# Performance work log

Hardware: AMD Instinct MI355X
Metric: run time of the kernel (lower is better)

The kernel has to match this reference:

```python
import jax, jax.numpy as jnp
import numpy as np

B_, L_, H_, P_ = 8, 4096, 512, 256
DT_MIN, DT_MAX = 1e-3, 1e-1


def setup_inputs() -> dict:
    key = jax.random.key(0)
    ks = jax.random.split(key, 6)
    input_sequence = jax.random.normal(ks[0], (B_, L_, H_), jnp.float32)
    # Stable diagonal SSM eigenvalues (HiPPO-like): negative real, spread imaginary
    Lambda_re = -0.5 * jnp.ones((P_,), jnp.float32)
    Lambda_im = jnp.pi * jnp.arange(P_, dtype=jnp.float32)
    # B, C stored as real arrays with trailing real/imag channel, as in the module
    B = jax.random.normal(ks[1], (P_, H_, 2), jnp.float32) / np.sqrt(2.0 * H_)
    C = jax.random.normal(ks[2], (H_, P_, 2), jnp.float32) / np.sqrt(float(P_))
    D = jax.random.normal(ks[3], (H_,), jnp.float32)
    log_step = jax.random.uniform(ks[4], (P_,), jnp.float32,
                                  float(np.log(DT_MIN)), float(np.log(DT_MAX)))
    return dict(input_sequence=input_sequence, Lambda_re=Lambda_re,
                Lambda_im=Lambda_im, B=B, C=C, D=D, log_step=log_step)


def _scan_ssm(Lambda_bar, Bu):
    """Diagonal linear recurrence x_k = Lambda_bar * x_{k-1} + Bu_k via parallel scan.
    Lambda_bar: (P,) complex64; Bu: (L, P) complex64 -> xs: (L, P) complex64."""
    A = jnp.broadcast_to(Lambda_bar, Bu.shape)

    def binop(e_i, e_j):
        a_i, b_i = e_i
        a_j, b_j = e_j
        return a_j * a_i, a_j * b_i + b_j

    _, xs = jax.lax.associative_scan(binop, (A, Bu))
    return xs


def reference(input_sequence, Lambda_re, Lambda_im, B, C, D, log_step):
    # complex parameters (conj_sym=True, clip_eigs=False, zoh discretization)
    Lambda = (Lambda_re + 1j * Lambda_im).astype(jnp.complex64)        # (P,)
    B_tilde = (B[..., 0] + 1j * B[..., 1]).astype(jnp.complex64)       # (P, H)
    C_tilde = (C[..., 0] + 1j * C[..., 1]).astype(jnp.complex64)       # (H, P)
    step = jnp.exp(log_step)                                           # (P,)
    # ZOH: Lambda_bar = exp(Lambda*dt); B_bar = Lambda^{-1}(Lambda_bar - I) B
    Lambda_bar = jnp.exp(Lambda * step)                                # (P,)
    B_bar = ((1.0 / Lambda) * (Lambda_bar - 1.0))[:, None] * B_tilde   # (P, H)
    # project inputs into state space: (B, L, P)
    Bu = jnp.einsum('blh,ph->blp', input_sequence.astype(jnp.complex64), B_bar)
    xs = jax.vmap(lambda bu: _scan_ssm(Lambda_bar, bu))(Bu)            # (B, L, P)
    state = xs[:, -1, :]                                               # (B, P)
    # conj_sym=True -> output uses 2 * Re(C x)
    ys = 2.0 * jnp.einsum('blp,hp->blh', xs, C_tilde).real             # (B, L, H)
    out = ys + D * input_sequence                                      # D-skip
    return out, state
```

## Files before the change

kernel.cpp:

```cpp
#include <hip/hip_runtime.h>
#include <hip/hip_bf16.h>

#define Hh 512
#define Pp 256
#define Ll 4096
#define Bb 8
#define BL (Bb*Ll)
#define Sc 64
#define NC 64

typedef __attribute__((ext_vector_type(8))) __bf16 bf16x8;
typedef __attribute__((ext_vector_type(4))) float  floatx4;

#define LAM_OFF     0
#define LAMS64D_OFF 512
#define B1G_OFF     1024
#define B3G_OFF     (B1G_OFF + 65536)
#define UB16_OFF    (B3G_OFF + 65536)
#define BUB_OFF     (UB16_OFF + 4194304)
#define XSB_OFF     (BUB_OFF + 4194304)
#define AGG_OFF     (XSB_OFF + 4194304)

#define OUT_ELEMS 16777216

#define GLL16(g, l) __builtin_amdgcn_global_load_lds( \
    (const __attribute__((address_space(1))) void*)(g), \
    (__attribute__((address_space(3))) void*)(l), 16, 0, 0)

#define BAR_LGKM()  asm volatile("s_waitcnt lgkmcnt(0)\n\ts_barrier" ::: "memory")
#define BAR_VMN(n)  asm volatile("s_waitcnt vmcnt(" #n ")\n\ts_barrier" ::: "memory")

__device__ __forceinline__ float2 cmul(float2 a, float2 b) {
    return make_float2(a.x*b.x - a.y*b.y, a.x*b.y + a.y*b.x);
}
__device__ __forceinline__ void cfma(float2& acc, float2 a, float2 b) {
    acc.x = fmaf(a.x, b.x, acc.x); acc.x = fmaf(-a.y, b.y, acc.x);
    acc.y = fmaf(a.x, b.y, acc.y); acc.y = fmaf( a.y, b.x, acc.y);
}

__global__ void prep(const float* __restrict__ u,
                     const float* __restrict__ Bmat, const float* __restrict__ Cmat,
                     const float* __restrict__ Lre, const float* __restrict__ Lim,
                     const float* __restrict__ logstep, float2* __restrict__ ws) {
    int bid = blockIdx.x;
    if (bid < 8192) {
        long i = ((long)bid * 256 + threadIdx.x) * 8;
        float4 v0 = *(const float4*)(u + i);
        float4 v1 = *(const float4*)(u + i + 4);
        __align__(16) __hip_bfloat162 t[4];
        t[0] = __float22bfloat162_rn(make_float2(v0.x, v0.y));
        t[1] = __float22bfloat162_rn(make_float2(v0.z, v0.w));
        t[2] = __float22bfloat162_rn(make_float2(v1.x, v1.y));
        t[3] = __float22bfloat162_rn(make_float2(v1.z, v1.w));
        *(bf16x8*)((__hip_bfloat16*)(ws + UB16_OFF) + i) = *(const bf16x8*)t;
    } else if (bid < 8704) {
        int idx = (bid - 8192) * 256 + threadIdx.x;
        int p = idx >> 9, h = idx & 511;
        double lr = (double)Lre[p], li = (double)Lim[p];
        double st = exp((double)logstep[p]);
        double a  = lr * st, th = li * st;
        double er = exp(a);
        double lamr = er * cos(th), lami = er * sin(th);
        double nr = lamr - 1.0, ni = lami;
        double den = lr*lr + li*li;
        float gx = (float)((nr*lr + ni*li)/den), gy = (float)((ni*lr - nr*li)/den);
        float2 b = ((const float2*)Bmat)[idx];
        float re = gx*b.x - gy*b.y;
        float im = gx*b.y + gy*b.x;
        __hip_bfloat16* B1 = (__hip_bfloat16*)(ws + B1G_OFF);
        B1[(2*p)*512 + h]   = __float2bfloat16(re);
        B1[(2*p+1)*512 + h] = __float2bfloat16(im);
    } else if (bid < 9216) {
        int idx = (bid - 8704) * 256 + threadIdx.x;
        int h = idx >> 8, p = idx & 255;
        float2 c = ((const float2*)Cmat)[idx];
        __hip_bfloat162* B3 = (__hip_bfloat162*)(ws + B3G_OFF);
        B3[h*256 + p] = __float22bfloat162_rn(make_float2(2.f*c.x, -2.f*c.y));
    } else {
        int p = threadIdx.x;
        double lr = (double)Lre[p], li = (double)Lim[p];
        double st = exp((double)logstep[p]);
        double a  = lr * st, th = li * st;
        double er = exp(a);
        ws[LAM_OFF + p] = make_float2((float)(er*cos(th)), (float)(er*sin(th)));
        double er64 = exp(64.0 * a), th64 = 64.0 * th;
        ((double2*)(ws + LAMS64D_OFF))[p] = make_double2(er64*cos(th64), er64*sin(th64));
    }
}

#define STAGE(buf, kt) do { \
    _Pragma("unroll") \
    for (int h_ = 0; h_ < 2; ++h_) { \
        _Pragma("unroll") \
        for (int r_ = 0; r_ < 2; ++r_) { \
            GLL16(aSrc + (h_*128 + r_*64)*1024 + (kt)*128, \
                  ldsSt + (buf)*65536 + h_*16384 + r_*8192); \
            GLL16(bSrc + (h_*128 + r_*64)*1024 + (kt)*128, \
                  ldsSt + (buf)*65536 + 32768 + h_*16384 + r_*8192); \
        } \
    } \
} while (0)

__global__ __launch_bounds__(512, 2)
void gemm1(const __hip_bfloat16* __restrict__ A,
           const __hip_bfloat16* __restrict__ B,
           void* __restrict__ Cout,
           const float2* __restrict__ lamTab,
           float2* __restrict__ aggOut) {
    __shared__ __align__(16) char lds[131072];
    const int tid = threadIdx.x;
    const int w = tid >> 6, l = tid & 63;

    const int idx = blockIdx.x;
    const int swz = (idx & 7) * 32 + (idx >> 3);
    const int mt = swz >> 1, nt = swz & 1;
    const long M0 = (long)mt * 256;
    const int  N0 = nt * 256;

    const int rA  = l >> 3;
    const int csw = ((l & 7) ^ rA) * 16;
    const char* aSrc = (const char*)A + (M0 + w*8 + rA) * 1024 + csw;
    const char* bSrc = (const char*)B + (long)(N0 + w*8 + rA) * 1024 + csw;
    char* ldsSt = lds + w*1024 + l*16;

    const int quad = l >> 4, ml = l & 15, m7 = ml & 7;
    const int wm = w & 1, wn = w >> 1;
    const int o0 = ((quad    ) ^ m7) * 16;
    const int o1 = ((quad + 4) ^ m7) * 16;
    const char* aRd = lds + wm*16384 + ml*128;
    const char* bRd = lds + 32768 + wn*8192 + ml*128;

    floatx4 acc[8][4];
    #pragma unroll
    for (int i = 0; i < 8; ++i)
        #pragma unroll
        for (int j = 0; j < 4; ++j) acc[i][j] = (floatx4)0.f;

    STAGE(0, 0);
    STAGE(1, 1);
    BAR_VMN(8);

    #pragma unroll
    for (int t = 0; t < 8; ++t) {
        const int tb = (t & 1) * 65536;
        {
            bf16x8 af[8], bfr[4];
            #pragma unroll
            for (int fm = 0; fm < 8; ++fm)
                af[fm] = *(const bf16x8*)(aRd + tb + fm*2048 + o0);
            #pragma unroll
            for (int fn = 0; fn < 4; ++fn)
                bfr[fn] = *(const bf16x8*)(bRd + tb + fn*2048 + o0);
            __builtin_amdgcn_s_setprio(1);
            #pragma unroll
            for (int fm = 0; fm < 8; ++fm)
                #pragma unroll
                for (int fn = 0; fn < 4; ++fn)
                    acc[fm][fn] = __builtin_amdgcn_mfma_f32_16x16x32_bf16(
                        af[fm], bfr[fn], acc[fm][fn], 0, 0, 0);
            __builtin_amdgcn_s_setprio(0);
        }
        {
            bf16x8 af[8], bfr[4];
            #pragma unroll
            for (int fm = 0; fm < 8; ++fm)
                af[fm] = *(const bf16x8*)(aRd + tb + fm*2048 + o1);
            #pragma unroll
            for (int fn = 0; fn < 4; ++fn)
                bfr[fn] = *(const bf16x8*)(bRd + tb + fn*2048 + o1);
            BAR_LGKM();
            if (t + 2 < 8) STAGE(t & 1, t + 2);
            __builtin_amdgcn_sched_barrier(0);
            __builtin_amdgcn_s_setprio(1);
            #pragma unroll
            for (int fm = 0; fm < 8; ++fm)
                #pragma unroll
                for (int fn = 0; fn < 4; ++fn)
                    acc[fm][fn] = __builtin_amdgcn_mfma_f32_16x16x32_bf16(
                        af[fm], bfr[fn], acc[fm][fn], 0, 0, 0);
            __builtin_amdgcn_s_setprio(0);
        }
        if (t < 6)       BAR_VMN(8);
        else if (t == 6) BAR_VMN(0);
    }

    const int b   = (int)(M0 >> 12);
    const int gc0 = (int)((M0 >> 6) & 63);
    #pragma unroll
    for (int fn = 0; fn < 4; ++fn) {
        const int col = N0 + wn*64 + fn*16 + ml;
        const int p = col >> 1;
        const float2 lam = lamTab[p];
        const float2 one = make_float2(1.f, 0.f);
        const float2 l2  = cmul(lam, lam);
        const float2 l3  = cmul(l2, lam);
        const float2 l4  = cmul(l2, l2);
        const float2 l8  = cmul(l4, l4);
        const float2 l12 = cmul(l8, l4);
        const float2 l16 = cmul(l8, l8);
        const float2 l32 = cmul(l16, l16);
        const float2 l48 = cmul(l32, l16);
        const float2 P4q = (quad==3) ? one : (quad==2) ? l4 : (quad==1) ? l8 : l12;
        #pragma unroll
        for (int c = 0; c < 2; ++c) {
            float2 sc = make_float2(0.f, 0.f);
            #pragma unroll
            for (int a = 0; a < 4; ++a) {
                const int fm = c*4 + a;
                float vr[4];
                #pragma unroll
                for (int reg = 0; reg < 4; ++reg) {
                    const long row = M0 + wm*128 + fm*16 + quad*4 + reg;
                    __hip_bfloat16 hv = __float2bfloat16(acc[fm][fn][reg]);
                    ((__hip_bfloat16*)Cout)[row * 512 + col] = hv;
                    vr[reg] = __bfloat162float(hv);
                }
                float2 s;
                s.x = fmaf(l3.x, vr[0], fmaf(l2.x, vr[1], fmaf(lam.x, vr[2], vr[3])));
                s.y = fmaf(l3.y, vr[0], fmaf(l2.y, vr[1], lam.y * vr[2]));
                const float2 p16 = (a==3) ? one : (a==2) ? l16 : (a==1) ? l32 : l48;
                cfma(sc, cmul(p16, P4q), s);
            }
            sc.x += __shfl_xor(sc.x, 16); sc.y += __shfl_xor(sc.y, 16);
            sc.x += __shfl_xor(sc.x, 32); sc.y += __shfl_xor(sc.y, 32);
            const float ox = __shfl_xor(sc.x, 1);
            const float oy = __shfl_xor(sc.y, 1);
            if (quad == 0 && (ml & 1) == 0) {
                aggOut[(b*NC + gc0 + wm*2 + c) * Pp + p] =
                    make_float2(sc.x - oy, sc.y + ox);
            }
        }
    }
}

#define STAGEB(buf, kt) do { \
    _Pragma("unroll") \
    for (int h_ = 0; h_ < 2; ++h_) { \
        _Pragma("unroll") \
        for (int r_ = 0; r_ < 2; ++r_) { \
            GLL16(bSrc + (h_*128 + r_*64)*1024 + (kt)*128, \
                  ldsB + (buf)*32768 + h_*16384 + r_*8192); \
        } \
    } \
} while (0)

__global__ __launch_bounds__(512, 2)
void gemm2f(const __hip_bfloat162* __restrict__ bub,
            const __hip_bfloat16* __restrict__ Bg,
            float* __restrict__ out,
            const __hip_bfloat16* __restrict__ ub,
            const float* __restrict__ Dv,
            const float2* __restrict__ lamTab,
            const double2* __restrict__ lam64,
            const float2* __restrict__ agg) {
    __shared__ __align__(16) char lds[139264];
    const int tid = threadIdx.x;
    const int w = tid >> 6, l = tid & 63;

    const int idx = blockIdx.x;
    const int swz = (idx & 7) * 32 + (idx >> 3);
    const int mt = swz >> 1, nt = swz & 1;
    const long M0 = (long)mt * 256;
    const int  N0 = nt * 256;
    const int b   = (int)(M0 >> 12);
    const int gc0 = (int)((M0 >> 6) & 63);

    const int rA  = l >> 3;
    const int csw = ((l & 7) ^ rA) * 16;
    const char* bSrc = (const char*)Bg + (long)(N0 + w*8 + rA) * 1024 + csw;
    char* ldsB = lds + 65536 + w*1024 + l*16;

    const int quad = l >> 4, ml = l & 15, m7 = ml & 7;
    const int wm = w & 1, wn = w >> 1;
    const int o0 = ((quad    ) ^ m7) * 16;
    const int o1 = ((quad + 4) ^ m7) * 16;
    const char* aRd = lds + wm*16384 + ml*128;
    const char* bRd = lds + 65536 + wn*8192 + ml*128;

    float2* carryL = (float2*)(lds + 131072);

    if (tid < 256) {
        const int p = tid;
        const double2 l64 = lam64[p];
        double cr = 0.0, ci = 0.0;
        for (int cp = 0; cp < gc0; ++cp) {
            float2 a = agg[(b*NC + cp) * Pp + p];
            double nr = fma(l64.x, cr, (double)a.x); nr = fma(-l64.y, ci, nr);
            double ni = fma(l64.x, ci, (double)a.y); ni = fma( l64.y, cr, ni);
            cr = nr; ci = ni;
        }
        carryL[0*256 + p] = make_float2((float)cr, (float)ci);
        #pragma unroll
        for (int i = 1; i < 4; ++i) {
            float2 a = agg[(b*NC + gc0 + i - 1) * Pp + p];
            double nr = fma(l64.x, cr, (double)a.x); nr = fma(-l64.y, ci, nr);
            double ni = fma(l64.x, ci, (double)a.y); ni = fma( l64.y, cr, ni);
            cr = nr; ci = ni;
            carryL[i*256 + p] = make_float2((float)cr, (float)ci);
        }
    }
    __syncthreads();

    floatx4 acc[8][4];
    #pragma unroll
    for (int i = 0; i < 8; ++i)
        #pragma unroll
        for (int j = 0; j < 4; ++j) acc[i][j] = (floatx4)0.f;

    auto scanTile = [&](int kt, int bufA) {
        if (tid < 128) {
            const int p5 = tid & 31, chunk = tid >> 5;
            const int p = kt*32 + p5;
            const float2 lam = lamTab[p];
            float2 x = carryL[chunk*256 + p];
            const __hip_bfloat162* src = bub + ((long)(M0 + chunk*64)) * 256 + p;
            char* abase = lds + bufA*32768 + (chunk*64)*128;
            const int cs = p5*4;
            for (int j0 = 0; j0 < 64; j0 += 8) {
                float2 v[8];
                #pragma unroll
                for (int i = 0; i < 8; ++i)
                    v[i] = __bfloat1622float2(src[(long)(j0 + i) * 256]);
                #pragma unroll
                for (int i = 0; i < 8; ++i) {
                    float nr = fmaf(lam.x, x.x, v[i].x); nr = fmaf(-lam.y, x.y, nr);
                    float ni = fmaf(lam.x, x.y, v[i].y); ni = fmaf( lam.y, x.x, ni);
                    x.x = nr; x.y = ni;
                    const int j = j0 + i;
                    *(__hip_bfloat162*)(abase + j*128 + (cs ^ ((j & 7) << 4))) =
                        __float22bfloat162_rn(x);
                }
            }
            if (gc0 == 60 && chunk == 3 && nt == 0) {
                out[OUT_ELEMS + b * Pp + p] = x.x;
                out[OUT_ELEMS + Bb * Pp + b * Pp + p] = x.y;
            }
        }
    };

    scanTile(0, 0);
    STAGEB(0, 0);
    __syncthreads();

    for (int kt = 0; kt < 8; ++kt) {
        const int cb = kt & 1;
        if (kt < 7) { scanTile(kt + 1, cb ^ 1); STAGEB(cb ^ 1, kt + 1); }
        __syncthreads();
        const int tb = cb * 32768;
        bf16x8 af[8], bfr[4];
        #pragma unroll
        for (int fm = 0; fm < 8; ++fm)
            af[fm] = *(const bf16x8*)(aRd + tb + fm*2048 + o0);
        #pragma unroll
        for (int fn = 0; fn < 4; ++fn)
            bfr[fn] = *(const bf16x8*)(bRd + tb + fn*2048 + o0);
        __builtin_amdgcn_s_setprio(1);
        #pragma unroll
        for (int fm = 0; fm < 8; ++fm)
            #pragma unroll
            for (int fn = 0; fn < 4; ++fn)
                acc[fm][fn] = __builtin_amdgcn_mfma_f32_16x16x32_bf16(
                    af[fm], bfr[fn], acc[fm][fn], 0, 0, 0);
        __builtin_amdgcn_s_setprio(0);
        #pragma unroll
        for (int fm = 0; fm < 8; ++fm)
            af[fm] = *(const bf16x8*)(aRd + tb + fm*2048 + o1);
        #pragma unroll
        for (int fn = 0; fn < 4; ++fn)
            bfr[fn] = *(const bf16x8*)(bRd + tb + fn*2048 + o1);
        __builtin_amdgcn_s_setprio(1);
        #pragma unroll
        for (int fm = 0; fm < 8; ++fm)
            #pragma unroll
            for (int fn = 0; fn < 4; ++fn)
                acc[fm][fn] = __builtin_amdgcn_mfma_f32_16x16x32_bf16(
                    af[fm], bfr[fn], acc[fm][fn], 0, 0, 0);
        __builtin_amdgcn_s_setprio(0);
        __syncthreads();
    }

    #pragma unroll
    for (int fm = 0; fm < 8; ++fm)
        #pragma unroll
        for (int fn = 0; fn < 4; ++fn) {
            const int col = N0 + wn*64 + fn*16 + ml;
            const float d = Dv[col];
            #pragma unroll
            for (int reg = 0; reg < 4; ++reg) {
                const long row = M0 + wm*128 + fm*16 + quad*4 + reg;
                const long o = row * 512 + col;
                out[o] = acc[fm][fn][reg] + d * __bfloat162float(ub[o]);
            }
        }
}

extern "C" void kernel_launch(void* const* d_in, const int* in_sizes, int n_in,
                              void* d_out, int out_size, void* d_ws, size_t ws_size,
                              hipStream_t stream) {
    const float* u       = (const float*)d_in[0];
    const float* Lre     = (const float*)d_in[1];
    const float* Lim     = (const float*)d_in[2];
    const float* Bmat    = (const float*)d_in[3];
    const float* Cmat    = (const float*)d_in[4];
    const float* Dv      = (const float*)d_in[5];
    const float* logstep = (const float*)d_in[6];
    float*  out = (float*)d_out;
    float2* ws  = (float2*)d_ws;

    prep<<<9217, 256, 0, stream>>>(u, Bmat, Cmat, Lre, Lim, logstep, ws);

    gemm1<<<256, 512, 0, stream>>>(
        (const __hip_bfloat16*)(ws + UB16_OFF),
        (const __hip_bfloat16*)(ws + B1G_OFF),
        (void*)(ws + BUB_OFF),
        (const float2*)(ws + LAM_OFF), (float2*)(ws + AGG_OFF));

    gemm2f<<<256, 512, 0, stream>>>(
        (const __hip_bfloat162*)(ws + BUB_OFF),
        (const __hip_bfloat16*)(ws + B3G_OFF),
        out,
        (const __hip_bfloat16*)(ws + UB16_OFF), Dv,
        (const float2*)(ws + LAM_OFF),
        (const double2*)(ws + LAMS64D_OFF),
        (const float2*)(ws + AGG_OFF));
}
```

Measured before the change: 196.6 us.

## Split scan into 16-step subchunks and async-stage Bu tiles in fused GEMM2

gemm1 now also emits per-16-row sub-chunk aggregates, and prep computes Lambda^16 in double. This lets gemm2f give the in-tile scan to all 512 threads, each handling 16 rows, instead of 128 threads each walking 64 rows. The Bu tiles are now loaded into LDS with async global-to-LDS copies two k-steps ahead, and the scan runs in place on LDS, replacing strided global reads by a few threads. This adds extra shuffles and stores in gemm1, more LDS use, and carry setup that depends on more aggregates.

```diff
diff --git a/kernel.cpp b/kernel.cpp
--- a/kernel.cpp
+++ b/kernel.cpp
@@ -20,6 +20,9 @@
 #define BUB_OFF     (UB16_OFF + 4194304)
 #define XSB_OFF     (BUB_OFF + 4194304)
 #define AGG_OFF     (XSB_OFF + 4194304)
+
+#define LAMS16D_OFF XSB_OFF
+#define AGG16_OFF   (XSB_OFF + 512)
 
 #define OUT_ELEMS 16777216
 
@@ -85,6 +88,8 @@
         ws[LAM_OFF + p] = make_float2((float)(er*cos(th)), (float)(er*sin(th)));
         double er64 = exp(64.0 * a), th64 = 64.0 * th;
         ((double2*)(ws + LAMS64D_OFF))[p] = make_double2(er64*cos(th64), er64*sin(th64));
+        double er16 = exp(16.0 * a), th16 = 16.0 * th;
+        ((double2*)(ws + LAMS16D_OFF))[p] = make_double2(er16*cos(th16), er16*sin(th16));
     }
 }
 
@@ -106,7 +111,8 @@
            const __hip_bfloat16* __restrict__ B,
            void* __restrict__ Cout,
            const float2* __restrict__ lamTab,
-           float2* __restrict__ aggOut) {
+           float2* __restrict__ aggOut,
+           float2* __restrict__ agg16Out) {
     __shared__ __align__(16) char lds[131072];
     const int tid = threadIdx.x;
     const int w = tid >> 6, l = tid & 63;
@@ -220,6 +226,14 @@
                 s.y = fmaf(l3.y, vr[0], fmaf(l2.y, vr[1], lam.y * vr[2]));
                 const float2 p16 = (a==3) ? one : (a==2) ? l16 : (a==1) ? l32 : l48;
                 cfma(sc, cmul(p16, P4q), s);
+                float2 tq = cmul(P4q, s);
+                tq.x += __shfl_xor(tq.x, 16); tq.y += __shfl_xor(tq.y, 16);
+                tq.x += __shfl_xor(tq.x, 32); tq.y += __shfl_xor(tq.y, 32);
+                const float tox = __shfl_xor(tq.x, 1);
+                const float toy = __shfl_xor(tq.y, 1);
+                if (quad == 0 && (ml & 1) == 0)
+                    agg16Out[((size_t)((b*NC + gc0 + wm*2 + c)*4 + a))*Pp + p] =
+                        make_float2(tq.x - toy, tq.y + tox);
             }
             sc.x += __shfl_xor(sc.x, 16); sc.y += __shfl_xor(sc.y, 16);
             sc.x += __shfl_xor(sc.x, 32); sc.y += __shfl_xor(sc.y, 32);
@@ -233,7 +247,17 @@
     }
 }
 
-#define STAGEB(buf, kt) do { \
+#define STAGEA2(buf, kt) do { \
+    _Pragma("unroll") \
+    for (int h_ = 0; h_ < 2; ++h_) { \
+        _Pragma("unroll") \
+        for (int r_ = 0; r_ < 2; ++r_) { \
+            GLL16(aSrc + (h_*128 + r_*64)*1024 + (kt)*128, \
+                  ldsA + (buf)*32768 + h_*16384 + r_*8192); \
+        } \
+    } \
+} while (0)
+#define STAGEB2(buf, kt) do { \
     _Pragma("unroll") \
     for (int h_ = 0; h_ < 2; ++h_) { \
         _Pragma("unroll") \
@@ -244,19 +268,41 @@
     } \
 } while (0)
 
+#define SCAN_TILE(ktC, bufA) do { \
+    const int s16_ = tid >> 5; \
+    const float2 lam_ = lamK[ktC]; \
+    float2 x_ = carry16L[s16_*256 + (ktC)*32 + p5g]; \
+    char* base_ = lds + (bufA)*32768; \
+    _Pragma("unroll") \
+    for (int jj_ = 0; jj_ < 16; ++jj_) { \
+        const int j_ = (s16_ << 4) + jj_; \
+        char* cell_ = base_ + j_*128 + ((((p5g >> 2) ^ (j_ & 7)) << 4) | ((p5g & 3) << 2)); \
+        float2 v_ = __bfloat1622float2(*(const __hip_bfloat162*)cell_); \
+        float nr_ = fmaf(lam_.x, x_.x, v_.x); nr_ = fmaf(-lam_.y, x_.y, nr_); \
+        float ni_ = fmaf(lam_.x, x_.y, v_.y); ni_ = fmaf( lam_.y, x_.x, ni_); \
+        x_.x = nr_; x_.y = ni_; \
+        *(__hip_bfloat162*)cell_ = __float22bfloat162_rn(x_); \
+    } \
+    if (s16_ == 15 && gc0 == 60 && nt == 0) { \
+        out[OUT_ELEMS + b * Pp + (ktC)*32 + p5g] = x_.x; \
+        out[OUT_ELEMS + Bb * Pp + b * Pp + (ktC)*32 + p5g] = x_.y; \
+    } \
+} while (0)
+
 __global__ __launch_bounds__(512, 2)
-void gemm2f(const __hip_bfloat162* __restrict__ bub,
+void gemm2f(const __hip_bfloat16* __restrict__ A,
             const __hip_bfloat16* __restrict__ Bg,
             float* __restrict__ out,
             const __hip_bfloat16* __restrict__ ub,
             const float* __restrict__ Dv,
             const float2* __restrict__ lamTab,
             const double2* __restrict__ lam64,
-            const float2* __restrict__ agg) {
-    __shared__ __align__(16) char lds[139264];
+            const double2* __restrict__ lam16,
+            const float2* __restrict__ agg,
+            const float2* __restrict__ agg16) {
+    __shared__ __align__(16) char lds[163840];
     const int tid = threadIdx.x;
     const int w = tid >> 6, l = tid & 63;
-
     const int idx = blockIdx.x;
     const int swz = (idx & 7) * 32 + (idx >> 3);
     const int mt = swz >> 1, nt = swz & 1;
@@ -267,7 +313,9 @@
 
     const int rA  = l >> 3;
     const int csw = ((l & 7) ^ rA) * 16;
+    const char* aSrc = (const char*)A + (M0 + w*8 + rA) * 1024 + csw;
     const char* bSrc = (const char*)Bg + (long)(N0 + w*8 + rA) * 1024 + csw;
+    char* ldsA = lds + w*1024 + l*16;
     char* ldsB = lds + 65536 + w*1024 + l*16;
 
     const int quad = l >> 4, ml = l & 15, m7 = ml & 7;
@@ -276,30 +324,59 @@
     const int o1 = ((quad + 4) ^ m7) * 16;
     const char* aRd = lds + wm*16384 + ml*128;
     const char* bRd = lds + 65536 + wn*8192 + ml*128;
-
-    float2* carryL = (float2*)(lds + 131072);
+    float2* carry16L = (float2*)(lds + 131072);
+
+    const int p5g = tid & 31;
+    float2 lamK[8];
+    #pragma unroll
+    for (int kt = 0; kt < 8; ++kt) lamK[kt] = lamTab[kt*32 + p5g];
+
+    STAGEA2(0, 0); STAGEB2(0, 0);
+    STAGEA2(1, 1); STAGEB2(1, 1);
 
     if (tid < 256) {
         const int p = tid;
         const double2 l64 = lam64[p];
+        const double2 l16 = lam16[p];
         double cr = 0.0, ci = 0.0;
-        for (int cp = 0; cp < gc0; ++cp) {
-            float2 a = agg[(b*NC + cp) * Pp + p];
-            double nr = fma(l64.x, cr, (double)a.x); nr = fma(-l64.y, ci, nr);
-            double ni = fma(l64.x, ci, (double)a.y); ni = fma( l64.y, cr, ni);
-            cr = nr; ci = ni;
-        }
-        carryL[0*256 + p] = make_float2((float)cr, (float)ci);
+        for (int cp = 0; cp + 4 <= gc0; cp += 4) {
+            float2 a0 = agg[(b*NC + cp    ) * Pp + p];
+            float2 a1 = agg[(b*NC + cp + 1) * Pp + p];
+            float2 a2 = agg[(b*NC + cp + 2) * Pp + p];
+            float2 a3 = agg[(b*NC + cp + 3) * Pp + p];
+            double nr, ni;
+            nr = fma(l64.x, cr, (double)a0.x); nr = fma(-l64.y, ci, nr);
+            ni = fma(l64.x, ci, (double)a0.y); ni = fma( l64.y, cr, ni); cr = nr; ci = ni;
+            nr = fma(l64.x, cr, (double)a1.x); nr = fma(-l64.y, ci, nr);
+            ni = fma(l64.x, ci, (double)a1.y); ni = fma( l64.y, cr, ni); cr = nr; ci = ni;
+            nr = fma(l64.x, cr, (double)a2.x); nr = fma(-l64.y, ci, nr);
+            ni = fma(l64.x, ci, (double)a2.y); ni = fma( l64.y, cr, ni); cr = nr; ci = ni;
+            nr = fma(l64.x, cr, (double)a3.x); nr = fma(-l64.y, ci, nr);
+            ni = fma(l64.x, ci, (double)a3.y); ni = fma( l64.y, cr, ni); cr = nr; ci = ni;
+        }
         #pragma unroll
-        for (int i = 1; i < 4; ++i) {
-            float2 a = agg[(b*NC + gc0 + i - 1) * Pp + p];
-            double nr = fma(l64.x, cr, (double)a.x); nr = fma(-l64.y, ci, nr);
-            double ni = fma(l64.x, ci, (double)a.y); ni = fma( l64.y, cr, ni);
-            cr = nr; ci = ni;
-            carryL[i*256 + p] = make_float2((float)cr, (float)ci);
+        for (int ch = 0; ch < 4; ++ch) {
+            carry16L[(ch*4 + 0)*256 + p] = make_float2((float)cr, (float)ci);
+            double scr = cr, sci = ci;
+            #pragma unroll
+            for (int sq = 1; sq < 4; ++sq) {
+                float2 a16 = agg16[((size_t)((b*NC + gc0 + ch)*4 + (sq-1)))*Pp + p];
+                double nr = fma(l16.x, scr, (double)a16.x); nr = fma(-l16.y, sci, nr);
+                double ni = fma(l16.x, sci, (double)a16.y); ni = fma( l16.y, scr, ni);
+                scr = nr; sci = ni;
+                carry16L[(ch*4 + sq)*256 + p] = make_float2((float)scr, (float)sci);
+            }
+            if (ch < 3) {
+                float2 a = agg[(b*NC + gc0 + ch) * Pp + p];
+                double nr = fma(l64.x, cr, (double)a.x); nr = fma(-l64.y, ci, nr);
+                double ni = fma(l64.x, ci, (double)a.y); ni = fma( l64.y, cr, ni);
+                cr = nr; ci = ni;
+            }
         }
     }
-    __syncthreads();
+    asm volatile("s_waitcnt vmcnt(8) lgkmcnt(0)\n\ts_barrier" ::: "memory");
+    SCAN_TILE(0, 0);
+    BAR_LGKM();
 
     floatx4 acc[8][4];
     #pragma unroll
@@ -307,76 +384,49 @@
         #pragma unroll
         for (int j = 0; j < 4; ++j) acc[i][j] = (floatx4)0.f;
 
-    auto scanTile = [&](int kt, int bufA) {
-        if (tid < 128) {
-            const int p5 = tid & 31, chunk = tid >> 5;
-            const int p = kt*32 + p5;
-            const float2 lam = lamTab[p];
-            float2 x = carryL[chunk*256 + p];
-            const __hip_bfloat162* src = bub + ((long)(M0 + chunk*64)) * 256 + p;
-            char* abase = lds + bufA*32768 + (chunk*64)*128;
-            const int cs = p5*4;
-            for (int j0 = 0; j0 < 64; j0 += 8) {
-                float2 v[8];
-                #pragma unroll
-                for (int i = 0; i < 8; ++i)
-                    v[i] = __bfloat1622float2(src[(long)(j0 + i) * 256]);
-                #pragma unroll
-                for (int i = 0; i < 8; ++i) {
-                    float nr = fmaf(lam.x, x.x, v[i].x); nr = fmaf(-lam.y, x.y, nr);
-                    float ni = fmaf(lam.x, x.y, v[i].y); ni = fmaf( lam.y, x.x, ni);
-                    x.x = nr; x.y = ni;
-                    const int j = j0 + i;
-                    *(__hip_bfloat162*)(abase + j*128 + (cs ^ ((j & 7) << 4))) =
-                        __float22bfloat162_rn(x);
-                }
-            }
-            if (gc0 == 60 && chunk == 3 && nt == 0) {
-                out[OUT_ELEMS + b * Pp + p] = x.x;
-                out[OUT_ELEMS + Bb * Pp + b * Pp + p] = x.y;
-            }
-        }
-    };
-
-    scanTile(0, 0);
-    STAGEB(0, 0);
-    __syncthreads();
-
+    #pragma unroll
     for (int kt = 0; kt < 8; ++kt) {
         const int cb = kt & 1;
-        if (kt < 7) { scanTile(kt + 1, cb ^ 1); STAGEB(cb ^ 1, kt + 1); }
-        __syncthreads();
         const int tb = cb * 32768;
-        bf16x8 af[8], bfr[4];
-        #pragma unroll
-        for (int fm = 0; fm < 8; ++fm)
-            af[fm] = *(const bf16x8*)(aRd + tb + fm*2048 + o0);
-        #pragma unroll
-        for (int fn = 0; fn < 4; ++fn)
-            bfr[fn] = *(const bf16x8*)(bRd + tb + fn*2048 + o0);
-        __builtin_amdgcn_s_setprio(1);
-        #pragma unroll
-        for (int fm = 0; fm < 8; ++fm)
+        {
+            bf16x8 af[8], bfr[4];
+            #pragma unroll
+            for (int fm = 0; fm < 8; ++fm)
+                af[fm] = *(const bf16x8*)(aRd + tb + fm*2048 + o0);
             #pragma unroll
             for (int fn = 0; fn < 4; ++fn)
-                acc[fm][fn] = __builtin_amdgcn_mfma_f32_16x16x32_bf16(
-                    af[fm], bfr[fn], acc[fm][fn], 0, 0, 0);
-        __builtin_amdgcn_s_setprio(0);
-        #pragma unroll
-        for (int fm = 0; fm < 8; ++fm)
-            af[fm] = *(const bf16x8*)(aRd + tb + fm*2048 + o1);
-        #pragma unroll
-        for (int fn = 0; fn < 4; ++fn)
-            bfr[fn] = *(const bf16x8*)(bRd + tb + fn*2048 + o1);
-        __builtin_amdgcn_s_setprio(1);
-        #pragma unroll
-        for (int fm = 0; fm < 8; ++fm)
+                bfr[fn] = *(const bf16x8*)(bRd + tb + fn*2048 + o0);
+            __builtin_amdgcn_s_setprio(1);
+            #pragma unroll
+            for (int fm = 0; fm < 8; ++fm)
+                #pragma unroll
+                for (int fn = 0; fn < 4; ++fn)
+                    acc[fm][fn] = __builtin_amdgcn_mfma_f32_16x16x32_bf16(
+                        af[fm], bfr[fn], acc[fm][fn], 0, 0, 0);
+            __builtin_amdgcn_s_setprio(0);
+        }
+        {
+            bf16x8 af[8], bfr[4];
+            #pragma unroll
+            for (int fm = 0; fm < 8; ++fm)
+                af[fm] = *(const bf16x8*)(aRd + tb + fm*2048 + o1);
             #pragma unroll
             for (int fn = 0; fn < 4; ++fn)
-                acc[fm][fn] = __builtin_amdgcn_mfma_f32_16x16x32_bf16(
-                    af[fm], bfr[fn], acc[fm][fn], 0, 0, 0);
-        __builtin_amdgcn_s_setprio(0);
-        __syncthreads();
+                bfr[fn] = *(const bf16x8*)(bRd + tb + fn*2048 + o1);
+            BAR_LGKM();
+            if (kt + 2 < 8) { STAGEA2(cb, kt + 2); STAGEB2(cb, kt + 2); }
+            __builtin_amdgcn_sched_barrier(0);
+            __builtin_amdgcn_s_setprio(1);
+            #pragma unroll
+            for (int fm = 0; fm < 8; ++fm)
+                #pragma unroll
+                for (int fn = 0; fn < 4; ++fn)
+                    acc[fm][fn] = __builtin_amdgcn_mfma_f32_16x16x32_bf16(
+                        af[fm], bfr[fn], acc[fm][fn], 0, 0, 0);
+            __builtin_amdgcn_s_setprio(0);
+        }
+        if (kt < 6)       { BAR_VMN(8); SCAN_TILE(kt + 1, cb ^ 1); BAR_LGKM(); }
+        else if (kt == 6) { BAR_VMN(0); SCAN_TILE(7, cb ^ 1); BAR_LGKM(); }
     }
 
     #pragma unroll
@@ -413,14 +463,18 @@
         (const __hip_bfloat16*)(ws + UB16_OFF),
         (const __hip_bfloat16*)(ws + B1G_OFF),
         (void*)(ws + BUB_OFF),
-        (const float2*)(ws + LAM_OFF), (float2*)(ws + AGG_OFF));
+        (const float2*)(ws + LAM_OFF),
+        (float2*)(ws + AGG_OFF),
+        (float2*)(ws + AGG16_OFF));
 
     gemm2f<<<256, 512, 0, stream>>>(
-        (const __hip_bfloat162*)(ws + BUB_OFF),
+        (const __hip_bfloat16*)(ws + BUB_OFF),
         (const __hip_bfloat16*)(ws + B3G_OFF),
         out,
         (const __hip_bfloat16*)(ws + UB16_OFF), Dv,
         (const float2*)(ws + LAM_OFF),
         (const double2*)(ws + LAMS64D_OFF),
-        (const float2*)(ws + AGG_OFF));
-}
+        (const double2*)(ws + LAMS16D_OFF),
+        (const float2*)(ws + AGG_OFF),
+        (const float2*)(ws + AGG16_OFF));
+}
```

Result: faster. 188.4 us (-4.2%).
